# Kernel tuning notes

Hardware: AMD Instinct MI355X
Metric: run time of the kernel (lower is better)

## Reference

```python
import jax, jax.numpy as jnp
import numpy as np

HEADS = 8
DIM_HEAD = 64
SCALE = DIM_HEAD ** -0.5
K = 7


def _conv(x, w, stride):
    return jax.lax.conv_general_dilated(
        x, w, window_strides=(stride, stride), padding='VALID',
        dimension_numbers=('NHWC', 'HWIO', 'NHWC'))


def _split_heads(t):
    # 'b x y (h d) -> (b h) (x y) d'
    b, X, Y, hd = t.shape
    d = hd // HEADS
    t = t.reshape(b, X, Y, HEADS, d)
    t = t.transpose(0, 3, 1, 2, 4)  # b h x y d
    return t.reshape(b * HEADS, X * Y, d)


def setup_inputs() -> dict:
    key = jax.random.key(0)
    ks = jax.random.split(key, 6)
    dim, inner = 256, HEADS * DIM_HEAD
    x = jax.random.normal(ks[0], (8, 84, 84, dim), dtype=jnp.float32)
    w_q = jax.random.normal(ks[1], (1, 1, dim, inner), dtype=jnp.float32) * 0.02
    w_kv = jax.random.normal(ks[2], (K, K, dim, 2 * inner), dtype=jnp.float32) * 0.02
    w_out = jax.random.normal(ks[3], (1, 1, inner, dim), dtype=jnp.float32) * 0.02
    b_out = jnp.zeros((dim,), dtype=jnp.float32)
    return {"x": x, "w_q": w_q, "w_kv": w_kv, "w_out": w_out, "b_out": b_out}


def reference(x, w_q, w_kv, w_out, b_out):
    b, X, Y, _ = x.shape
    q = _conv(x, w_q, 1)          # [b, X, Y, inner]
    kv = _conv(x, w_kv, K)        # [b, X/k, Y/k, 2*inner]
    k, v = jnp.split(kv, 2, axis=-1)
    q = _split_heads(q)           # [(b h), XY, d]
    k = _split_heads(k)           # [(b h), xy, d]
    v = _split_heads(v)
    dots = jnp.einsum('bid,bjd->bij', q, k) * SCALE
    attn = jax.nn.softmax(dots, axis=-1)
    out = jnp.einsum('bij,bjd->bid', attn, v)  # [(b h), XY, d]
    out = out.reshape(b, HEADS, X, Y, DIM_HEAD).transpose(0, 2, 3, 1, 4)
    out = out.reshape(b, X, Y, HEADS * DIM_HEAD)
    out = _conv(out, w_out, 1) + b_out  # dropout rate 0 -> identity
    return out
```

## Files before the change

kernel.cpp:

```cpp
#include <hip/hip_runtime.h>

typedef unsigned short u16;
typedef __bf16 bf16x8 __attribute__((ext_vector_type(8)));
typedef __bf16 bf16x4 __attribute__((ext_vector_type(4)));
typedef float f32x4 __attribute__((ext_vector_type(4)));

__device__ __forceinline__ u16 f2b(float f) {
    __bf16 h = (__bf16)f;
    return __builtin_bit_cast(u16, h);
}
__device__ __forceinline__ unsigned pk2(float a, float b) {
    return (unsigned)f2b(a) | ((unsigned)f2b(b) << 16);
}

__device__ __forceinline__ int xcd_chunk(int wg, int n) {
    int q = n >> 3, r = n & 7;
    int x = wg & 7, i = wg >> 3;
    return (x < r ? x * (q + 1) : r * (q + 1) + (x - r) * q) + i;
}

#define GLOAD_LDS16(src, dst)                                              \
    __builtin_amdgcn_global_load_lds(                                      \
        (const __attribute__((address_space(1))) void*)(src),              \
        (__attribute__((address_space(3))) void*)(dst), 16, 0, 0)

__global__ __launch_bounds__(256) void k_pack_x(const float* __restrict__ x,
                                                u16* __restrict__ xp) {
    int v = blockIdx.x * 256 + threadIdx.x;
    int c0 = (v & 31) << 3;
    int pix = v >> 5;
    int b = pix / 7056;
    int r = pix - b * 7056;
    int y = r / 84;
    int xx = r - y * 84;
    int opix = (b * 144 + (y / 7) * 12 + (xx / 7)) * 49 + (y % 7) * 7 + (xx % 7);
    const float4* src = reinterpret_cast<const float4*>(x + ((size_t)pix << 8) + c0);
    float4 f0 = src[0], f1 = src[1];
    bf16x8 o = {(__bf16)f0.x, (__bf16)f0.y, (__bf16)f0.z, (__bf16)f0.w,
                (__bf16)f1.x, (__bf16)f1.y, (__bf16)f1.z, (__bf16)f1.w};
    *reinterpret_cast<bf16x8*>(xp + ((size_t)opix << 8) + c0) = o;
}

__global__ __launch_bounds__(256) void k_tconv(const float* __restrict__ in,
                                               u16* __restrict__ out, int R, int C,
                                               float scale, int permk) {
    __shared__ float tile[32][33];
    int c0 = blockIdx.x << 5, r0 = blockIdx.y << 5;
    int tx = threadIdx.x, ty = threadIdx.y;
#pragma unroll
    for (int i = 0; i < 4; i++)
        tile[ty + (i << 3)][tx] = in[(size_t)(r0 + ty + (i << 3)) * C + c0 + tx];
    __syncthreads();
    int k = r0 + tx;
    int kw = permk ? ((k & ~63) | ((k & 15) << 2) | ((k >> 4) & 3)) : k;
#pragma unroll
    for (int i = 0; i < 4; i++)
        out[(size_t)(c0 + ty + (i << 3)) * R + kw] = f2b(tile[tx][ty + (i << 3)] * scale);
}

__global__ __launch_bounds__(256) void k_kvproj(const u16* __restrict__ xp,
                                                const u16* __restrict__ wkvT,
                                                float* __restrict__ parts) {
    __shared__ u16 As[8192];
    __shared__ u16 Bs[4096];
    const int lin = xcd_chunk(blockIdx.x, 1008);
    const int mt = lin % 9;
    const int rest = lin / 9;
    const int nt = rest & 15;
    const int sp = rest >> 4;
    const int tid = threadIdx.x;
    const int wave = tid >> 6, lane = tid & 63;
    const int wr = wave >> 1, wc = wave & 1;
    const int lrow = lane & 15, lkg = lane >> 4;
    const u16* Ag = xp + (size_t)(mt * 128) * 12544 + sp * 1792;
    const u16* Bg = wkvT + (size_t)(nt * 64) * 12544 + sp * 1792;
    const int srow = lane >> 3;
    const int scol_sw = (((lane & 7) ^ srow) << 3);
    f32x4 acc[4][2];
#pragma unroll
    for (int m = 0; m < 4; m++)
#pragma unroll
        for (int n = 0; n < 2; n++)
#pragma unroll
            for (int i = 0; i < 4; i++) acc[m][n][i] = 0.f;

    for (int ks = 0; ks < 28; ks++) {
        const int k0 = ks << 6;
        __syncthreads();
#pragma unroll
        for (int j = 0; j < 4; j++) {
            const int c = (wave << 2) + j;
            const int row = (c << 3) + srow;
            GLOAD_LDS16(Ag + (size_t)row * 12544 + k0 + scol_sw, As + (c << 9));
        }
#pragma unroll
        for (int j = 0; j < 2; j++) {
            const int c = (wave << 1) + j;
            const int row = (c << 3) + srow;
            GLOAD_LDS16(Bg + (size_t)row * 12544 + k0 + scol_sw, Bs + (c << 9));
        }
        __syncthreads();
#pragma unroll
        for (int kk = 0; kk < 2; kk++) {
            const int sig = (kk << 2) + lkg;
            const int sw = ((sig ^ (lrow & 7)) << 3);
            bf16x8 a[4], bb[2];
#pragma unroll
            for (int m = 0; m < 4; m++)
                a[m] = *reinterpret_cast<const bf16x8*>(As + (((wr << 6) + (m << 4) + lrow) << 6) + sw);
#pragma unroll
            for (int n = 0; n < 2; n++)
                bb[n] = *reinterpret_cast<const bf16x8*>(Bs + (((wc << 5) + (n << 4) + lrow) << 6) + sw);
#pragma unroll
            for (int m = 0; m < 4; m++)
#pragma unroll
                for (int n = 0; n < 2; n++)
                    acc[m][n] = __builtin_amdgcn_mfma_f32_16x16x32_bf16(a[m], bb[n], acc[m][n], 0, 0, 0);
        }
    }
    float* outp = parts + (size_t)sp * 1179648;
#pragma unroll
    for (int m = 0; m < 4; m++)
#pragma unroll
        for (int n = 0; n < 2; n++)
#pragma unroll
            for (int i = 0; i < 4; i++) {
                int row = (mt << 7) + (wr << 6) + (m << 4) + (lkg << 2) + i;
                int col = (nt << 6) + (wc << 5) + (n << 4) + lrow;
                outp[(size_t)row * 1024 + col] = acc[m][n][i];
            }
}

__global__ __launch_bounds__(256) void k_kvfin(const float* __restrict__ parts,
                                               u16* __restrict__ Kf, u16* __restrict__ Vf) {
    int v = blockIdx.x * 256 + threadIdx.x;
    int m = v >> 8;
    int n0 = (v & 255) << 2;
    float4 s = {0.f, 0.f, 0.f, 0.f};
#pragma unroll
    for (int sp = 0; sp < 7; sp++) {
        float4 p = *reinterpret_cast<const float4*>(parts + (size_t)sp * 1179648 +
                                                    (size_t)m * 1024 + n0);
        s.x += p.x; s.y += p.y; s.z += p.z; s.w += p.w;
    }
    int b = m / 144, pi = m - b * 144;
    float sv[4] = {s.x, s.y, s.z, s.w};
#pragma unroll
    for (int e4 = 0; e4 < 4; e4++) {
        int n = n0 + e4;
        int h = (n & 511) >> 6, d = n & 63;
        int bh = (b << 3) + h;
        if (n < 512) {
            int fc = pi >> 4, lr = pi & 15;
            int ks = d >> 5, lg = (d >> 3) & 3, e = d & 7;
            Kf[((((size_t)bh * 9 + fc) << 1) + ks) * 512 + (((lg << 4) + lr) << 3) + e] = f2b(sv[e4]);
        } else {
            int nf = d >> 4, lr = d & 15;
            int ks = pi >> 5;
            int e = (((pi >> 4) & 1) << 2) | (pi & 3);
            int lg = (pi >> 2) & 3;
            Vf[(((size_t)bh * 4 + nf) * 5 + ks) * 512 + (((lg << 4) + lr) << 3) + e] = f2b(sv[e4]);
        }
    }
}

__global__ __launch_bounds__(256) void k_qproj(const u16* __restrict__ xp,
                                               const u16* __restrict__ wqT,
                                               u16* __restrict__ Qf) {
    __shared__ u16 As[128][72];
    __shared__ u16 Bs[128][72];
    const int lin = xcd_chunk(blockIdx.x, 1764);
    const int nt = lin & 3, mt = lin >> 2;
    const int tid = threadIdx.x;
    const int wave = tid >> 6, lane = tid & 63;
    const int wr = wave >> 1, wc = wave & 1;
    const int lrow = lane & 15, lkg = lane >> 4;
    const u16* Ag = xp + (size_t)(mt * 128) * 256;
    const u16* Bg = wqT + (size_t)(nt * 128) * 256;
    const int srow = tid >> 3, scol = (tid & 7) << 3;
    f32x4 acc[4][4];
#pragma unroll
    for (int m = 0; m < 4; m++)
#pragma unroll
        for (int n = 0; n < 4; n++)
#pragma unroll
            for (int i = 0; i < 4; i++) acc[m][n][i] = 0.f;

    for (int ks = 0; ks < 4; ks++) {
        const int k0 = ks * 64;
        __syncthreads();
#pragma unroll
        for (int p = 0; p < 4; p++) {
            int rr = srow + (p << 5);
            *reinterpret_cast<bf16x8*>(&As[rr][scol]) =
                *reinterpret_cast<const bf16x8*>(Ag + (size_t)rr * 256 + k0 + scol);
            *reinterpret_cast<bf16x8*>(&Bs[rr][scol]) =
                *reinterpret_cast<const bf16x8*>(Bg + (size_t)rr * 256 + k0 + scol);
        }
        __syncthreads();
#pragma unroll
        for (int kk = 0; kk < 2; kk++) {
            const int ko = (kk << 5) + (lkg << 3);
            bf16x8 a[4], bb[4];
#pragma unroll
            for (int m = 0; m < 4; m++)
                a[m] = *reinterpret_cast<const bf16x8*>(&As[(wr << 6) + (m << 4) + lrow][ko]);
#pragma unroll
            for (int n = 0; n < 4; n++)
                bb[n] = *reinterpret_cast<const bf16x8*>(&Bs[(wc << 6) + (n << 4) + lrow][ko]);
#pragma unroll
            for (int m = 0; m < 4; m++)
#pragma unroll
                for (int n = 0; n < 4; n++)
                    acc[m][n] = __builtin_amdgcn_mfma_f32_16x16x32_bf16(a[m], bb[n], acc[m][n], 0, 0, 0);
        }
    }
#pragma unroll
    for (int m = 0; m < 4; m++)
#pragma unroll
        for (int n = 0; n < 4; n++)
#pragma unroll
            for (int i = 0; i < 4; i++) {
                int row = (mt << 7) + (wr << 6) + (m << 4) + (lkg << 2) + i;
                int col = (nt << 7) + (wc << 6) + (n << 4) + lrow;
                int b = row / 7056, pp = row - b * 7056;
                int h = col >> 6, d = col & 63;
                int bh = (b << 3) + h;
                int tt = pp >> 4, flr = pp & 15;
                int fks = d >> 5, flg = (d >> 3) & 3, fe = d & 7;
                Qf[((((size_t)bh * 441 + tt) << 1) + fks) * 512 + (((flg << 4) + flr) << 3) + fe] =
                    f2b(acc[m][n][i]);
            }
}

__global__ __launch_bounds__(128, 4) void k_attn(const u16* __restrict__ Qf,
                                                 const u16* __restrict__ Kf,
                                                 const u16* __restrict__ Vf,
                                                 u16* __restrict__ O) {
    const int wv = threadIdx.x >> 6, lane = threadIdx.x & 63;
    const int t = blockIdx.x;
    const int h = (blockIdx.y << 1) + wv;
    const int b = blockIdx.z;
    const int lrow = lane & 15, lkg = lane >> 4;
    const int bh = (b << 3) + h;
    const int l8 = lane << 3;

    const u16* Qg = Qf + ((((size_t)bh * 441 + t) << 1) << 9);
    const u16* Kg = Kf + (((size_t)bh * 9) << 10);
    const u16* Vg = Vf + ((size_t)bh * 20) * 512;

    f32x4 da[9];
#pragma unroll
    for (int fc = 0; fc < 9; fc++)
#pragma unroll
        for (int i = 0; i < 4; i++) da[fc][i] = 0.f;
#pragma unroll
    for (int ks = 0; ks < 2; ks++) {
        bf16x8 aq = *reinterpret_cast<const bf16x8*>(Qg + (ks << 9) + l8);
#pragma unroll
        for (int fc = 0; fc < 9; fc++) {
            bf16x8 bk = *reinterpret_cast<const bf16x8*>(Kg + ((((fc << 1) + ks)) << 9) + l8);
            da[fc] = __builtin_amdgcn_mfma_f32_16x16x32_bf16(bk, aq, da[fc], 0, 0, 0);
        }
    }

    float mx = -1e30f;
#pragma unroll
    for (int fc = 0; fc < 9; fc++)
#pragma unroll
        for (int i = 0; i < 4; i++) mx = fmaxf(mx, da[fc][i]);
    mx = fmaxf(mx, __shfl_xor(mx, 16));
    mx = fmaxf(mx, __shfl_xor(mx, 32));
    float sum = 0.f;
#pragma unroll
    for (int fc = 0; fc < 9; fc++)
#pragma unroll
        for (int i = 0; i < 4; i++) {
            float v = __expf(da[fc][i] - mx);
            da[fc][i] = v;
            sum += v;
        }
    sum += __shfl_xor(sum, 16);
    sum += __shfl_xor(sum, 32);
    float inv = 1.0f / sum;
    unsigned pw[9][2];
#pragma unroll
    for (int fc = 0; fc < 9; fc++) {
        pw[fc][0] = pk2(da[fc][0] * inv, da[fc][1] * inv);
        pw[fc][1] = pk2(da[fc][2] * inv, da[fc][3] * inv);
    }

    f32x4 oa[4];
#pragma unroll
    for (int n = 0; n < 4; n++)
#pragma unroll
        for (int i = 0; i < 4; i++) oa[n][i] = 0.f;
#pragma unroll
    for (int ks = 0; ks < 5; ks++) {
        uint4 pav;
        if (ks < 4)
            pav = uint4{pw[2 * ks][0], pw[2 * ks][1], pw[2 * ks + 1][0], pw[2 * ks + 1][1]};
        else
            pav = uint4{pw[8][0], pw[8][1], 0u, 0u};
        bf16x8 pa = __builtin_bit_cast(bf16x8, pav);
#pragma unroll
        for (int n = 0; n < 4; n++) {
            bf16x8 bv = *reinterpret_cast<const bf16x8*>(Vg + ((size_t)(n * 5 + ks) << 9) + l8);
            oa[n] = __builtin_amdgcn_mfma_f32_16x16x32_bf16(pa, bv, oa[n], 0, 0, 0);
        }
    }

#pragma unroll
    for (int i = 0; i < 4; i++) {
        int r = (lkg << 2) + i;
        int q = (t << 4) + r;
        int pi = q / 49, pos = q - pi * 49;
        int y = (pi / 12) * 7 + pos / 7;
        int xx = (pi - (pi / 12) * 12) * 7 + (pos - (pos / 7) * 7);
        bf16x4 ov = {(__bf16)oa[0][i], (__bf16)oa[1][i], (__bf16)oa[2][i], (__bf16)oa[3][i]};
        *reinterpret_cast<bf16x4*>(O + (((size_t)b * 7056 + y * 84 + xx) << 9) +
                                   (h << 6) + (lrow << 2)) = ov;
    }
}

__global__ __launch_bounds__(256) void k_outproj(const u16* __restrict__ A,
                                                 const u16* __restrict__ BT,
                                                 const float* __restrict__ bias,
                                                 float* __restrict__ out) {
    __shared__ u16 As[128][72];
    __shared__ u16 Bs[128][72];
    const int lin = xcd_chunk(blockIdx.x, 882);
    const int nt = lin & 1, mt = lin >> 1;
    const int tid = threadIdx.x;
    const int wave = tid >> 6, lane = tid & 63;
    const int wr = wave >> 1, wc = wave & 1;
    const int lrow = lane & 15, lkg = lane >> 4;
    const u16* Ag = A + (size_t)(mt * 128) * 512;
    const u16* Bg = BT + (size_t)(nt * 128) * 512;
    const int srow = tid >> 3, scol = (tid & 7) << 3;
    f32x4 acc[4][4];
#pragma unroll
    for (int m = 0; m < 4; m++)
#pragma unroll
        for (int n = 0; n < 4; n++)
#pragma unroll
            for (int i = 0; i < 4; i++) acc[m][n][i] = 0.f;

    for (int ks = 0; ks < 8; ks++) {
        const int k0 = ks * 64;
        __syncthreads();
#pragma unroll
        for (int p = 0; p < 4; p++) {
            int rr = srow + (p << 5);
            *reinterpret_cast<bf16x8*>(&As[rr][scol]) =
                *reinterpret_cast<const bf16x8*>(Ag + (size_t)rr * 512 + k0 + scol);
            *reinterpret_cast<bf16x8*>(&Bs[rr][scol]) =
                *reinterpret_cast<const bf16x8*>(Bg + (size_t)rr * 512 + k0 + scol);
        }
        __syncthreads();
#pragma unroll
        for (int kk = 0; kk < 2; kk++) {
            const int ko = (kk << 5) + (lkg << 3);
            bf16x8 a[4], bb[4];
#pragma unroll
            for (int m = 0; m < 4; m++)
                a[m] = *reinterpret_cast<const bf16x8*>(&As[(wr << 6) + (m << 4) + lrow][ko]);
#pragma unroll
            for (int n = 0; n < 4; n++)
                bb[n] = *reinterpret_cast<const bf16x8*>(&Bs[(wc << 6) + (n << 4) + lrow][ko]);
#pragma unroll
            for (int m = 0; m < 4; m++)
#pragma unroll
                for (int n = 0; n < 4; n++)
                    acc[m][n] = __builtin_amdgcn_mfma_f32_16x16x32_bf16(a[m], bb[n], acc[m][n], 0, 0, 0);
        }
    }
#pragma unroll
    for (int m = 0; m < 4; m++)
#pragma unroll
        for (int n = 0; n < 4; n++)
#pragma unroll
            for (int i = 0; i < 4; i++) {
                int row = (mt << 7) + (wr << 6) + (m << 4) + (lkg << 2) + i;
                int col = (nt << 7) + (wc << 6) + (n << 4) + lrow;
                out[(size_t)row * 256 + col] = acc[m][n][i] + bias[col];
            }
}

extern "C" void kernel_launch(void* const* d_in, const int* in_sizes, int n_in,
                              void* d_out, int out_size, void* d_ws, size_t ws_size,
                              hipStream_t stream) {
    const float* x = (const float*)d_in[0];
    const float* w_q = (const float*)d_in[1];
    const float* w_kv = (const float*)d_in[2];
    const float* w_out = (const float*)d_in[3];
    const float* b_out = (const float*)d_in[4];
    float* out = (float*)d_out;

    char* ws = (char*)d_ws;
    size_t off = 0;
    auto alloc = [&](size_t bytes) -> char* {
        char* p = ws + off;
        off = (off + bytes + 255) & ~(size_t)255;
        return p;
    };
    u16* xp = (u16*)alloc(28901376ull);
    u16* wqT = (u16*)alloc(262144ull);
    u16* woutT = (u16*)alloc(262144ull);
    u16* Kf = (u16*)alloc(1179648ull);
    u16* Vf = (u16*)alloc(1310720ull);
    u16* O = (u16*)alloc(57802752ull);
    u16* wkvT = (u16*)alloc(25690112ull);
    float* parts = (float*)alloc(33030144ull);
    u16* Qf = (u16*)wkvT;

    hipMemsetAsync(Vf, 0, 1310720ull, stream);
    k_pack_x<<<7056, 256, 0, stream>>>(x, xp);
    k_tconv<<<dim3(32, 392), dim3(32, 8), 0, stream>>>(w_kv, wkvT, 12544, 1024, 1.0f, 0);
    k_tconv<<<dim3(16, 8), dim3(32, 8), 0, stream>>>(w_q, wqT, 256, 512, 0.125f, 0);
    k_tconv<<<dim3(8, 16), dim3(32, 8), 0, stream>>>(w_out, woutT, 512, 256, 1.0f, 1);
    k_kvproj<<<1008, 256, 0, stream>>>(xp, wkvT, parts);
    k_kvfin<<<1152, 256, 0, stream>>>(parts, Kf, Vf);
    k_qproj<<<1764, 256, 0, stream>>>(xp, wqT, Qf);
    k_attn<<<dim3(441, 4, 8), 128, 0, stream>>>(Qf, Kf, Vf, O);
    k_outproj<<<882, 256, 0, stream>>>(O, woutT, b_out, out);
}
```

Baseline: 223.3 us.

## Double-buffer kvproj LDS tiles and give each attention wave several query tiles

The kv-projection GEMM now uses two LDS buffers, so the global-to-LDS load of the next K slice is issued before computing the current one, with one barrier per iteration instead of two. The attention kernel changes its grid: each 192-thread block handles one head with three waves, and each wave loops over three consecutive query tiles. This reuses K/V for a head within the block and cuts block count and launch overhead. The costs are doubled LDS use in kvproj, which may lower occupancy, and a different occupancy target for attention.

```diff
diff --git a/kernel.cpp b/kernel.cpp
--- a/kernel.cpp
+++ b/kernel.cpp
@@ -61,8 +61,8 @@
 __global__ __launch_bounds__(256) void k_kvproj(const u16* __restrict__ xp,
                                                 const u16* __restrict__ wkvT,
                                                 float* __restrict__ parts) {
-    __shared__ u16 As[8192];
-    __shared__ u16 Bs[4096];
+    __shared__ u16 As[2][8192];
+    __shared__ u16 Bs[2][4096];
     const int lin = xcd_chunk(blockIdx.x, 1008);
     const int mt = lin % 9;
     const int rest = lin / 9;
@@ -76,30 +76,36 @@
     const u16* Bg = wkvT + (size_t)(nt * 64) * 12544 + sp * 1792;
     const int srow = lane >> 3;
     const int scol_sw = (((lane & 7) ^ srow) << 3);
-    f32x4 acc[4][2];
-#pragma unroll
-    for (int m = 0; m < 4; m++)
-#pragma unroll
-        for (int n = 0; n < 2; n++)
-#pragma unroll
-            for (int i = 0; i < 4; i++) acc[m][n][i] = 0.f;
-
-    for (int ks = 0; ks < 28; ks++) {
+
+    auto stage = [&](int buf, int ks) {
         const int k0 = ks << 6;
-        __syncthreads();
 #pragma unroll
         for (int j = 0; j < 4; j++) {
             const int c = (wave << 2) + j;
             const int row = (c << 3) + srow;
-            GLOAD_LDS16(Ag + (size_t)row * 12544 + k0 + scol_sw, As + (c << 9));
+            GLOAD_LDS16(Ag + (size_t)row * 12544 + k0 + scol_sw, &As[buf][c << 9]);
         }
 #pragma unroll
         for (int j = 0; j < 2; j++) {
             const int c = (wave << 1) + j;
             const int row = (c << 3) + srow;
-            GLOAD_LDS16(Bg + (size_t)row * 12544 + k0 + scol_sw, Bs + (c << 9));
-        }
-        __syncthreads();
+            GLOAD_LDS16(Bg + (size_t)row * 12544 + k0 + scol_sw, &Bs[buf][c << 9]);
+        }
+    };
+
+    f32x4 acc[4][2];
+#pragma unroll
+    for (int m = 0; m < 4; m++)
+#pragma unroll
+        for (int n = 0; n < 2; n++)
+#pragma unroll
+            for (int i = 0; i < 4; i++) acc[m][n][i] = 0.f;
+
+    stage(0, 0);
+    __syncthreads();
+    for (int ks = 0; ks < 28; ks++) {
+        const int cur = ks & 1;
+        if (ks < 27) stage(cur ^ 1, ks + 1);
 #pragma unroll
         for (int kk = 0; kk < 2; kk++) {
             const int sig = (kk << 2) + lkg;
@@ -107,16 +113,17 @@
             bf16x8 a[4], bb[2];
 #pragma unroll
             for (int m = 0; m < 4; m++)
-                a[m] = *reinterpret_cast<const bf16x8*>(As + (((wr << 6) + (m << 4) + lrow) << 6) + sw);
+                a[m] = *reinterpret_cast<const bf16x8*>(&As[cur][(((wr << 6) + (m << 4) + lrow) << 6) + sw]);
 #pragma unroll
             for (int n = 0; n < 2; n++)
-                bb[n] = *reinterpret_cast<const bf16x8*>(Bs + (((wc << 5) + (n << 4) + lrow) << 6) + sw);
+                bb[n] = *reinterpret_cast<const bf16x8*>(&Bs[cur][(((wc << 5) + (n << 4) + lrow) << 6) + sw]);
 #pragma unroll
             for (int m = 0; m < 4; m++)
 #pragma unroll
                 for (int n = 0; n < 2; n++)
                     acc[m][n] = __builtin_amdgcn_mfma_f32_16x16x32_bf16(a[m], bb[n], acc[m][n], 0, 0, 0);
         }
+        __syncthreads();
     }
     float* outp = parts + (size_t)sp * 1179648;
 #pragma unroll
@@ -233,93 +240,97 @@
             }
 }
 
-__global__ __launch_bounds__(128, 4) void k_attn(const u16* __restrict__ Qf,
+__global__ __launch_bounds__(192, 7) void k_attn(const u16* __restrict__ Qf,
                                                  const u16* __restrict__ Kf,
                                                  const u16* __restrict__ Vf,
                                                  u16* __restrict__ O) {
     const int wv = threadIdx.x >> 6, lane = threadIdx.x & 63;
-    const int t = blockIdx.x;
-    const int h = (blockIdx.y << 1) + wv;
-    const int b = blockIdx.z;
+    const int h = blockIdx.y, b = blockIdx.z;
     const int lrow = lane & 15, lkg = lane >> 4;
     const int bh = (b << 3) + h;
     const int l8 = lane << 3;
 
-    const u16* Qg = Qf + ((((size_t)bh * 441 + t) << 1) << 9);
     const u16* Kg = Kf + (((size_t)bh * 9) << 10);
     const u16* Vg = Vf + ((size_t)bh * 20) * 512;
-
-    f32x4 da[9];
-#pragma unroll
-    for (int fc = 0; fc < 9; fc++)
-#pragma unroll
-        for (int i = 0; i < 4; i++) da[fc][i] = 0.f;
-#pragma unroll
-    for (int ks = 0; ks < 2; ks++) {
-        bf16x8 aq = *reinterpret_cast<const bf16x8*>(Qg + (ks << 9) + l8);
+    const int t0 = (blockIdx.x * 3 + wv) * 3;
+
+#pragma unroll 1
+    for (int j = 0; j < 3; j++) {
+        const int t = t0 + j;
+        const u16* Qg = Qf + (((size_t)bh * 441 + t) << 10);
+
+        f32x4 da[9];
+#pragma unroll
+        for (int fc = 0; fc < 9; fc++)
+#pragma unroll
+            for (int i = 0; i < 4; i++) da[fc][i] = 0.f;
+#pragma unroll
+        for (int ks = 0; ks < 2; ks++) {
+            bf16x8 aq = *reinterpret_cast<const bf16x8*>(Qg + (ks << 9) + l8);
+#pragma unroll
+            for (int fc = 0; fc < 9; fc++) {
+                bf16x8 bk = *reinterpret_cast<const bf16x8*>(Kg + ((((fc << 1) + ks)) << 9) + l8);
+                da[fc] = __builtin_amdgcn_mfma_f32_16x16x32_bf16(bk, aq, da[fc], 0, 0, 0);
+            }
+        }
+
+        float mx = -1e30f;
+#pragma unroll
+        for (int fc = 0; fc < 9; fc++)
+#pragma unroll
+            for (int i = 0; i < 4; i++) mx = fmaxf(mx, da[fc][i]);
+        mx = fmaxf(mx, __shfl_xor(mx, 16));
+        mx = fmaxf(mx, __shfl_xor(mx, 32));
+        float sum = 0.f;
+#pragma unroll
+        for (int fc = 0; fc < 9; fc++)
+#pragma unroll
+            for (int i = 0; i < 4; i++) {
+                float vv = __expf(da[fc][i] - mx);
+                da[fc][i] = vv;
+                sum += vv;
+            }
+        sum += __shfl_xor(sum, 16);
+        sum += __shfl_xor(sum, 32);
+        float inv = 1.0f / sum;
+        unsigned pw[9][2];
 #pragma unroll
         for (int fc = 0; fc < 9; fc++) {
-            bf16x8 bk = *reinterpret_cast<const bf16x8*>(Kg + ((((fc << 1) + ks)) << 9) + l8);
-            da[fc] = __builtin_amdgcn_mfma_f32_16x16x32_bf16(bk, aq, da[fc], 0, 0, 0);
-        }
-    }
-
-    float mx = -1e30f;
-#pragma unroll
-    for (int fc = 0; fc < 9; fc++)
-#pragma unroll
-        for (int i = 0; i < 4; i++) mx = fmaxf(mx, da[fc][i]);
-    mx = fmaxf(mx, __shfl_xor(mx, 16));
-    mx = fmaxf(mx, __shfl_xor(mx, 32));
-    float sum = 0.f;
-#pragma unroll
-    for (int fc = 0; fc < 9; fc++)
+            pw[fc][0] = pk2(da[fc][0] * inv, da[fc][1] * inv);
+            pw[fc][1] = pk2(da[fc][2] * inv, da[fc][3] * inv);
+        }
+
+        f32x4 oa[4];
+#pragma unroll
+        for (int n = 0; n < 4; n++)
+#pragma unroll
+            for (int i = 0; i < 4; i++) oa[n][i] = 0.f;
+#pragma unroll
+        for (int ks = 0; ks < 5; ks++) {
+            uint4 pav;
+            if (ks < 4)
+                pav = uint4{pw[2 * ks][0], pw[2 * ks][1], pw[2 * ks + 1][0], pw[2 * ks + 1][1]};
+            else
+                pav = uint4{pw[8][0], pw[8][1], 0u, 0u};
+            bf16x8 pa = __builtin_bit_cast(bf16x8, pav);
+#pragma unroll
+            for (int n = 0; n < 4; n++) {
+                bf16x8 bv = *reinterpret_cast<const bf16x8*>(Vg + ((size_t)(n * 5 + ks) << 9) + l8);
+                oa[n] = __builtin_amdgcn_mfma_f32_16x16x32_bf16(pa, bv, oa[n], 0, 0, 0);
+            }
+        }
+
 #pragma unroll
         for (int i = 0; i < 4; i++) {
-            float v = __expf(da[fc][i] - mx);
-            da[fc][i] = v;
-            sum += v;
-        }
-    sum += __shfl_xor(sum, 16);
-    sum += __shfl_xor(sum, 32);
-    float inv = 1.0f / sum;
-    unsigned pw[9][2];
-#pragma unroll
-    for (int fc = 0; fc < 9; fc++) {
-        pw[fc][0] = pk2(da[fc][0] * inv, da[fc][1] * inv);
-        pw[fc][1] = pk2(da[fc][2] * inv, da[fc][3] * inv);
-    }
-
-    f32x4 oa[4];
-#pragma unroll
-    for (int n = 0; n < 4; n++)
-#pragma unroll
-        for (int i = 0; i < 4; i++) oa[n][i] = 0.f;
-#pragma unroll
-    for (int ks = 0; ks < 5; ks++) {
-        uint4 pav;
-        if (ks < 4)
-            pav = uint4{pw[2 * ks][0], pw[2 * ks][1], pw[2 * ks + 1][0], pw[2 * ks + 1][1]};
-        else
-            pav = uint4{pw[8][0], pw[8][1], 0u, 0u};
-        bf16x8 pa = __builtin_bit_cast(bf16x8, pav);
-#pragma unroll
-        for (int n = 0; n < 4; n++) {
-            bf16x8 bv = *reinterpret_cast<const bf16x8*>(Vg + ((size_t)(n * 5 + ks) << 9) + l8);
-            oa[n] = __builtin_amdgcn_mfma_f32_16x16x32_bf16(pa, bv, oa[n], 0, 0, 0);
-        }
-    }
-
-#pragma unroll
-    for (int i = 0; i < 4; i++) {
-        int r = (lkg << 2) + i;
-        int q = (t << 4) + r;
-        int pi = q / 49, pos = q - pi * 49;
-        int y = (pi / 12) * 7 + pos / 7;
-        int xx = (pi - (pi / 12) * 12) * 7 + (pos - (pos / 7) * 7);
-        bf16x4 ov = {(__bf16)oa[0][i], (__bf16)oa[1][i], (__bf16)oa[2][i], (__bf16)oa[3][i]};
-        *reinterpret_cast<bf16x4*>(O + (((size_t)b * 7056 + y * 84 + xx) << 9) +
-                                   (h << 6) + (lrow << 2)) = ov;
+            int r = (lkg << 2) + i;
+            int q = (t << 4) + r;
+            int pi = q / 49, pos = q - pi * 49;
+            int y = (pi / 12) * 7 + pos / 7;
+            int xx = (pi - (pi / 12) * 12) * 7 + (pos - (pos / 7) * 7);
+            bf16x4 ov = {(__bf16)oa[0][i], (__bf16)oa[1][i], (__bf16)oa[2][i], (__bf16)oa[3][i]};
+            *reinterpret_cast<bf16x4*>(O + (((size_t)b * 7056 + y * 84 + xx) << 9) +
+                                       (h << 6) + (lrow << 2)) = ov;
+        }
     }
 }
 
@@ -422,6 +433,6 @@
     k_kvproj<<<1008, 256, 0, stream>>>(xp, wkvT, parts);
     k_kvfin<<<1152, 256, 0, stream>>>(parts, Kf, Vf);
     k_qproj<<<1764, 256, 0, stream>>>(xp, wqT, Qf);
-    k_attn<<<dim3(441, 4, 8), 128, 0, stream>>>(Qf, Kf, Vf, O);
+    k_attn<<<dim3(49, 8, 8), 192, 0, stream>>>(Qf, Kf, Vf, O);
     k_outproj<<<882, 256, 0, stream>>>(O, woutT, b_out, out);
 }
```

New measurement: 491.7 us. 120% more time.

## Double-buffer LDS tiles in kv-projection and out-projection GEMMs

Applied to the files above, without the earlier changes.

Both the kv-projection and output-projection GEMM kernels now use two LDS buffers and prefetch the next K-slice while computing on the current one. This cuts the loop to one barrier per step and overlaps global loads with MFMA work. The out-projection also switches from register-staged copies to direct global-to-LDS loads with an XOR swizzle in place of padding, and uses 32-wide K steps. The cost is twice the LDS per block, which may reduce occupancy.

```diff
diff --git a/kernel.cpp b/kernel.cpp
--- a/kernel.cpp
+++ b/kernel.cpp
@@ -61,8 +61,8 @@
 __global__ __launch_bounds__(256) void k_kvproj(const u16* __restrict__ xp,
                                                 const u16* __restrict__ wkvT,
                                                 float* __restrict__ parts) {
-    __shared__ u16 As[8192];
-    __shared__ u16 Bs[4096];
+    __shared__ u16 As[2][8192];
+    __shared__ u16 Bs[2][4096];
     const int lin = xcd_chunk(blockIdx.x, 1008);
     const int mt = lin % 9;
     const int rest = lin / 9;
@@ -76,30 +76,36 @@
     const u16* Bg = wkvT + (size_t)(nt * 64) * 12544 + sp * 1792;
     const int srow = lane >> 3;
     const int scol_sw = (((lane & 7) ^ srow) << 3);
-    f32x4 acc[4][2];
-#pragma unroll
-    for (int m = 0; m < 4; m++)
-#pragma unroll
-        for (int n = 0; n < 2; n++)
-#pragma unroll
-            for (int i = 0; i < 4; i++) acc[m][n][i] = 0.f;
-
-    for (int ks = 0; ks < 28; ks++) {
+
+    auto stage = [&](int buf, int ks) {
         const int k0 = ks << 6;
-        __syncthreads();
 #pragma unroll
         for (int j = 0; j < 4; j++) {
             const int c = (wave << 2) + j;
             const int row = (c << 3) + srow;
-            GLOAD_LDS16(Ag + (size_t)row * 12544 + k0 + scol_sw, As + (c << 9));
+            GLOAD_LDS16(Ag + (size_t)row * 12544 + k0 + scol_sw, &As[buf][c << 9]);
         }
 #pragma unroll
         for (int j = 0; j < 2; j++) {
             const int c = (wave << 1) + j;
             const int row = (c << 3) + srow;
-            GLOAD_LDS16(Bg + (size_t)row * 12544 + k0 + scol_sw, Bs + (c << 9));
-        }
-        __syncthreads();
+            GLOAD_LDS16(Bg + (size_t)row * 12544 + k0 + scol_sw, &Bs[buf][c << 9]);
+        }
+    };
+
+    f32x4 acc[4][2];
+#pragma unroll
+    for (int m = 0; m < 4; m++)
+#pragma unroll
+        for (int n = 0; n < 2; n++)
+#pragma unroll
+            for (int i = 0; i < 4; i++) acc[m][n][i] = 0.f;
+
+    stage(0, 0);
+    __syncthreads();
+    for (int ks = 0; ks < 28; ks++) {
+        const int cur = ks & 1;
+        if (ks < 27) stage(cur ^ 1, ks + 1);
 #pragma unroll
         for (int kk = 0; kk < 2; kk++) {
             const int sig = (kk << 2) + lkg;
@@ -107,16 +113,17 @@
             bf16x8 a[4], bb[2];
 #pragma unroll
             for (int m = 0; m < 4; m++)
-                a[m] = *reinterpret_cast<const bf16x8*>(As + (((wr << 6) + (m << 4) + lrow) << 6) + sw);
+                a[m] = *reinterpret_cast<const bf16x8*>(&As[cur][(((wr << 6) + (m << 4) + lrow) << 6) + sw]);
 #pragma unroll
             for (int n = 0; n < 2; n++)
-                bb[n] = *reinterpret_cast<const bf16x8*>(Bs + (((wc << 5) + (n << 4) + lrow) << 6) + sw);
+                bb[n] = *reinterpret_cast<const bf16x8*>(&Bs[cur][(((wc << 5) + (n << 4) + lrow) << 6) + sw]);
 #pragma unroll
             for (int m = 0; m < 4; m++)
 #pragma unroll
                 for (int n = 0; n < 2; n++)
                     acc[m][n] = __builtin_amdgcn_mfma_f32_16x16x32_bf16(a[m], bb[n], acc[m][n], 0, 0, 0);
         }
+        __syncthreads();
     }
     float* outp = parts + (size_t)sp * 1179648;
 #pragma unroll
@@ -327,8 +334,8 @@
                                                  const u16* __restrict__ BT,
                                                  const float* __restrict__ bias,
                                                  float* __restrict__ out) {
-    __shared__ u16 As[128][72];
-    __shared__ u16 Bs[128][72];
+    __shared__ u16 As[2][4096];
+    __shared__ u16 Bs[2][4096];
     const int lin = xcd_chunk(blockIdx.x, 882);
     const int nt = lin & 1, mt = lin >> 1;
     const int tid = threadIdx.x;
@@ -337,7 +344,20 @@
     const int lrow = lane & 15, lkg = lane >> 4;
     const u16* Ag = A + (size_t)(mt * 128) * 512;
     const u16* Bg = BT + (size_t)(nt * 128) * 512;
-    const int srow = tid >> 3, scol = (tid & 7) << 3;
+    const int srow16 = lane >> 2;
+    const int sslot = (((lane & 3) ^ (srow16 & 3)) << 3);
+
+    auto stage = [&](int buf, int ks) {
+        const int k0 = ks << 5;
+#pragma unroll
+        for (int j = 0; j < 2; j++) {
+            const int c = (wave << 1) + j;
+            const int row = (c << 4) + srow16;
+            GLOAD_LDS16(Ag + (size_t)row * 512 + k0 + sslot, &As[buf][c << 9]);
+            GLOAD_LDS16(Bg + (size_t)row * 512 + k0 + sslot, &Bs[buf][c << 9]);
+        }
+    };
+
     f32x4 acc[4][4];
 #pragma unroll
     for (int m = 0; m < 4; m++)
@@ -346,34 +366,29 @@
 #pragma unroll
             for (int i = 0; i < 4; i++) acc[m][n][i] = 0.f;
 
-    for (int ks = 0; ks < 8; ks++) {
-        const int k0 = ks * 64;
+    stage(0, 0);
+    __syncthreads();
+    const int rslot = ((lkg ^ (lrow & 3)) << 3);
+    for (int ks = 0; ks < 16; ks++) {
+        const int cur = ks & 1;
+        if (ks < 15) stage(cur ^ 1, ks + 1);
+        bf16x8 a[4], bb[4];
+#pragma unroll
+        for (int m = 0; m < 4; m++) {
+            int r = (wr << 6) + (m << 4) + lrow;
+            a[m] = *reinterpret_cast<const bf16x8*>(&As[cur][(r << 5) + rslot]);
+        }
+#pragma unroll
+        for (int n = 0; n < 4; n++) {
+            int r = (wc << 6) + (n << 4) + lrow;
+            bb[n] = *reinterpret_cast<const bf16x8*>(&Bs[cur][(r << 5) + rslot]);
+        }
+#pragma unroll
+        for (int m = 0; m < 4; m++)
+#pragma unroll
+            for (int n = 0; n < 4; n++)
+                acc[m][n] = __builtin_amdgcn_mfma_f32_16x16x32_bf16(a[m], bb[n], acc[m][n], 0, 0, 0);
         __syncthreads();
-#pragma unroll
-        for (int p = 0; p < 4; p++) {
-            int rr = srow + (p << 5);
-            *reinterpret_cast<bf16x8*>(&As[rr][scol]) =
-                *reinterpret_cast<const bf16x8*>(Ag + (size_t)rr * 512 + k0 + scol);
-            *reinterpret_cast<bf16x8*>(&Bs[rr][scol]) =
-                *reinterpret_cast<const bf16x8*>(Bg + (size_t)rr * 512 + k0 + scol);
-        }
-        __syncthreads();
-#pragma unroll
-        for (int kk = 0; kk < 2; kk++) {
-            const int ko = (kk << 5) + (lkg << 3);
-            bf16x8 a[4], bb[4];
-#pragma unroll
-            for (int m = 0; m < 4; m++)
-                a[m] = *reinterpret_cast<const bf16x8*>(&As[(wr << 6) + (m << 4) + lrow][ko]);
-#pragma unroll
-            for (int n = 0; n < 4; n++)
-                bb[n] = *reinterpret_cast<const bf16x8*>(&Bs[(wc << 6) + (n << 4) + lrow][ko]);
-#pragma unroll
-            for (int m = 0; m < 4; m++)
-#pragma unroll
-                for (int n = 0; n < 4; n++)
-                    acc[m][n] = __builtin_amdgcn_mfma_f32_16x16x32_bf16(a[m], bb[n], acc[m][n], 0, 0, 0);
-        }
     }
 #pragma unroll
     for (int m = 0; m < 4; m++)
```

New measurement: 233.5 us. 1.05x slower.
